# Optimization experiments

Measured on AMD Instinct MI355X. Metric: run time of the kernel, lower is better.

Reference implementation:

```python
import jax, jax.numpy as jnp
import numpy as np

E = 500000       # number of temporal edges
D = 128          # in_feats
DOUT = 128       # out_feats
N_NODES = 50000  # destination node vocabulary


def setup_inputs() -> dict:
    key = jax.random.key(0)
    k = jax.random.split(key, 6)
    src_feat = jax.random.normal(k[0], (E, D), jnp.float32)
    dst_feat = jax.random.normal(k[1], (E, D), jnp.float32)
    # edges sorted by destination node (and implicitly by timestamp within each bucket)
    dst = jnp.sort(jax.random.randint(k[2], (E,), 0, N_NODES))
    W_self = jax.random.normal(k[3], (D, DOUT), jnp.float32) / np.sqrt(D).astype(np.float32)
    b_self = jnp.zeros((DOUT,), jnp.float32)
    W_neigh = jax.random.normal(k[4], (D, DOUT), jnp.float32) / np.sqrt(D).astype(np.float32)
    b_neigh = jnp.zeros((DOUT,), jnp.float32)
    return dict(src_feat=src_feat, dst_feat=dst_feat, dst=dst,
                W_self=W_self, b_self=b_self, W_neigh=W_neigh, b_neigh=b_neigh)


def _segment_cummean(feat, dst):
    """Cumulative mean of `feat` within contiguous buckets of equal `dst`.

    Equivalent to DGL group_apply_edges(group_by='dst') with the 'mean' branch:
    h_feat = cumsum(h_neighs, dim=1) / (deg_index + 1) on the ragged buckets.
    """
    En = feat.shape[0]
    idx = jnp.arange(En)
    is_start = jnp.concatenate([jnp.ones((1,), bool), dst[1:] != dst[:-1]])
    # running max propagates each bucket's start index to all of its edges
    start_idx = jax.lax.associative_scan(jnp.maximum, jnp.where(is_start, idx, 0))
    cs = jnp.cumsum(feat, axis=0)  # [E, D] global prefix sum
    base = jnp.where((start_idx > 0)[:, None],
                     cs[jnp.maximum(start_idx - 1, 0)], jnp.float32(0.0))
    seg_cs = cs - base                       # within-bucket inclusive cumsum
    pos = (idx - start_idx).astype(feat.dtype)
    return seg_cs / (pos + 1.0)[:, None]     # cumulative mean


def reference(src_feat, dst_feat, dst, W_self, b_self, W_neigh, b_neigh):
    h_neigh = _segment_cummean(src_feat, dst)
    # rst = fc_self(h_self) + fc_neigh(mask_feat)
    return (dst_feat @ W_self + b_self) + (h_neigh @ W_neigh + b_neigh)
```

## Files before the change

kernel.cpp:

```cpp
#include <hip/hip_runtime.h>

typedef float f32x4 __attribute__((ext_vector_type(4)));
typedef __bf16 bf16x8 __attribute__((ext_vector_type(8)));

typedef __attribute__((address_space(3))) unsigned char lds_u8;
typedef __attribute__((address_space(1))) const unsigned char g_u8c;

__device__ __forceinline__ unsigned short f2bf(float f) {
  unsigned int u = __float_as_uint(f);
  u += 0x7FFFu + ((u >> 16) & 1u);
  return (unsigned short)(u >> 16);
}
__device__ __forceinline__ unsigned int pk2(float a, float b) {
  return (unsigned int)f2bf(a) | ((unsigned int)f2bf(b) << 16);
}
__device__ __forceinline__ void gload16(const void* g, void* l) {
  __builtin_amdgcn_global_load_lds((g_u8c*)g, (lds_u8*)l, 16, 0, 0);
}

__global__ void k_prep(const float* __restrict__ Ws, const float* __restrict__ Wn,
                       const float* __restrict__ bs, const float* __restrict__ bn,
                       unsigned short* __restrict__ wt, float* __restrict__ bias) {
  int idx = blockIdx.x * 256 + threadIdx.x;
  int n = idx >> 8, k = idx & 255;
  float v = (k < 128) ? Ws[k * 128 + n] : Wn[(k - 128) * 128 + n];
  int ct = n >> 4, l15 = n & 15, kt = k >> 5, lg = (k >> 3) & 3, j = k & 7;
  wt[(((kt << 3) | ct) << 9) + (((lg << 4) | l15) << 3) + j] = f2bf(v);
  if (idx < 128) bias[idx] = bs[idx] + bn[idx];
}

__global__ __launch_bounds__(128, 4) void k_fused(
    const float* __restrict__ src, const float* __restrict__ dstf,
    const int* __restrict__ dst, const unsigned short* __restrict__ wt,
    const float* __restrict__ bias, float* __restrict__ out, int E)
{
  __shared__ __align__(16) unsigned char slab[2][16384];
  const int lane = threadIdx.x & 63, wid = threadIdx.x >> 6;
  const int l15 = lane & 15, lg = lane >> 4;

  const int nwg = gridDim.x, bid = blockIdx.x;
  const int q = nwg >> 3, r = nwg & 7;
  const int xcd = bid & 7, ix = bid >> 3;
  const int swb = (xcd < r ? xcd * (q + 1) : r * (q + 1) + (xcd - r) * q) + ix;

  const long e0 = ((long)swb * 2 + wid) * 16;
  if (e0 >= E) return;
  const long emax = (long)E - 1;
  unsigned char* ssrc = slab[wid];
  unsigned char* sdst = slab[wid] + 8192;

  long drow = e0 + l15; if (drow > emax) drow = emax;
  int myd = dst[drow];
  long back = e0 - 1 - lane;
  long backc = back < 0 ? 0 : back;
  int bd = dst[backc];

  #pragma unroll
  for (int i = 0; i < 8; ++i) {
    int r2 = i * 2 + (lane >> 5);
    long gr = e0 + r2; if (gr > emax) gr = emax;
    int colb = ((lane & 31) << 4) ^ ((r2 & 7) << 5);
    gload16((const char*)src + gr * 512 + colb, ssrc + i * 1024);
  }
  #pragma unroll
  for (int i = 0; i < 8; ++i) {
    int r2 = i * 2 + (lane >> 5);
    long gr = e0 + r2; if (gr > emax) gr = emax;
    int colb = ((lane & 31) << 4) ^ ((r2 & 7) << 5);
    gload16((const char*)dstf + gr * 512 + colb, sdst + i * 1024);
  }

  int d0 = __shfl(myd, 0);
  unsigned long long m = __ballot((back >= 0) && (bd == d0));
  unsigned long long nm = ~m;
  int L = (nm == 0ull) ? 64 : __builtin_ctzll(nm);
  long s = e0 - L;
  while (s > 0 && dst[s - 1] == d0) --s;

  float ax = 0.f, ay = 0.f;
  for (long e = s; e < e0; ++e) {
    float2 v = *(const float2*)(src + e * 128 + lane * 2);
    ax += v.x; ay += v.y;
  }

  asm volatile("s_waitcnt vmcnt(8)" ::: "memory");

  int pos = (int)(e0 - s);
  int prevd = d0;
  #pragma unroll
  for (int rr = 0; rr < 16; ++rr) {
    int d = __shfl(myd, rr);
    if (d != prevd) { ax = 0.f; ay = 0.f; pos = 0; prevd = d; }
    float2 v = *(const float2*)(ssrc + rr * 512 + ((lane * 8) ^ ((rr & 7) << 5)));
    ax += v.x; ay += v.y;
    float inv = __builtin_amdgcn_rcpf((float)(pos + 1));
    *(unsigned int*)(ssrc + rr * 512 + ((lane * 4) ^ ((rr & 7) << 4))) = pk2(ax * inv, ay * inv);
    ++pos;
  }

  asm volatile("s_waitcnt lgkmcnt(0)" ::: "memory");
  asm volatile("s_waitcnt vmcnt(0)" ::: "memory");

  f32x4 acc[8];
  #pragma unroll
  for (int ct = 0; ct < 8; ++ct) acc[ct] = (f32x4){0.f, 0.f, 0.f, 0.f};
  float bcol[8];
  #pragma unroll
  for (int ct = 0; ct < 8; ++ct) bcol[ct] = bias[ct * 16 + l15];

  #pragma unroll
  for (int kt = 0; kt < 8; ++kt) {
    bf16x8 a;
    if (kt < 4) {
      const unsigned char* p = sdst + l15 * 512 + ((kt * 128 + lg * 32) ^ ((l15 & 7) << 5));
      float4 x = *(const float4*)p;
      float4 y = *(const float4*)(p + 16);
      union { unsigned int u[4]; bf16x8 v; } cv;
      cv.u[0] = pk2(x.x, x.y); cv.u[1] = pk2(x.z, x.w);
      cv.u[2] = pk2(y.x, y.y); cv.u[3] = pk2(y.z, y.w);
      a = cv.v;
    } else {
      a = *(const bf16x8*)(ssrc + l15 * 512 + ((((kt - 4) * 64) + lg * 16) ^ ((l15 & 7) << 4)));
    }
    bf16x8 b[8];
    #pragma unroll
    for (int ct = 0; ct < 8; ++ct)
      b[ct] = *(const bf16x8*)(wt + (((kt << 3) | ct) << 9) + (lane << 3));
    #pragma unroll
    for (int ct = 0; ct < 8; ++ct)
      acc[ct] = __builtin_amdgcn_mfma_f32_16x16x32_bf16(a, b[ct], acc[ct], 0, 0, 0);
  }

  #pragma unroll
  for (int i = 0; i < 4; ++i) {
    long row = e0 + lg * 4 + i;
    if (row < E) {
      float* op = out + row * 128 + l15;
      #pragma unroll
      for (int ct = 0; ct < 8; ++ct) op[ct * 16] = acc[ct][i] + bcol[ct];
    }
  }
}

extern "C" void kernel_launch(void* const* d_in, const int* in_sizes, int n_in,
                              void* d_out, int out_size, void* d_ws, size_t ws_size,
                              hipStream_t stream) {
  const float* src_feat = (const float*)d_in[0];
  const float* dst_feat = (const float*)d_in[1];
  const int*   dst      = (const int*)d_in[2];
  const float* W_self   = (const float*)d_in[3];
  const float* b_self   = (const float*)d_in[4];
  const float* W_neigh  = (const float*)d_in[5];
  const float* b_neigh  = (const float*)d_in[6];
  float* out = (float*)d_out;
  const int E = in_sizes[2];

  unsigned short* wt   = (unsigned short*)d_ws;
  float*          bias = (float*)((char*)d_ws + 65536);

  k_prep<<<128, 256, 0, stream>>>(W_self, W_neigh, b_self, b_neigh, wt, bias);

  int blocks = (E + 31) / 32;
  k_fused<<<blocks, 128, 0, stream>>>(src_feat, dst_feat, dst, wt, bias, out, E);
}
```

Measured before the change: 190.5 us.

## Load dst features directly to registers, widen blocks, batch backward prefix loads

Drops the LDS staging of dst_feat rows and loads them straight from global memory into registers just before the MFMA loop. This halves LDS per wave and allows 4 waves per 256-thread block. Bucket-boundary detection becomes a precomputed 16-bit ballot mask instead of per-row shuffles, and the backward prefix accumulation issues loads in batches of eight. In exchange, the dst_feat global loads no longer overlap with the cumulative-mean phase and are read in a less coalesced per-lane pattern, with a full vmcnt(0) wait placed earlier.

```diff
diff --git a/kernel.cpp b/kernel.cpp
--- a/kernel.cpp
+++ b/kernel.cpp
@@ -29,12 +29,12 @@
   if (idx < 128) bias[idx] = bs[idx] + bn[idx];
 }
 
-__global__ __launch_bounds__(128, 4) void k_fused(
+__global__ __launch_bounds__(256, 4) void k_fused(
     const float* __restrict__ src, const float* __restrict__ dstf,
     const int* __restrict__ dst, const unsigned short* __restrict__ wt,
     const float* __restrict__ bias, float* __restrict__ out, int E)
 {
-  __shared__ __align__(16) unsigned char slab[2][16384];
+  __shared__ __align__(16) unsigned char slab[4][8192];
   const int lane = threadIdx.x & 63, wid = threadIdx.x >> 6;
   const int l15 = lane & 15, lg = lane >> 4;
 
@@ -43,14 +43,15 @@
   const int xcd = bid & 7, ix = bid >> 3;
   const int swb = (xcd < r ? xcd * (q + 1) : r * (q + 1) + (xcd - r) * q) + ix;
 
-  const long e0 = ((long)swb * 2 + wid) * 16;
+  const long e0 = ((long)swb * 4 + wid) * 16;
   if (e0 >= E) return;
   const long emax = (long)E - 1;
   unsigned char* ssrc = slab[wid];
-  unsigned char* sdst = slab[wid] + 8192;
 
-  long drow = e0 + l15; if (drow > emax) drow = emax;
-  int myd = dst[drow];
+  long rc = e0 + l15; if (rc > emax) rc = emax;
+  int dcur = dst[rc];
+  long rp = rc - 1; if (rp < 0) rp = 0;
+  int dprev = dst[rp];
   long back = e0 - 1 - lane;
   long backc = back < 0 ? 0 : back;
   int bd = dst[backc];
@@ -62,15 +63,10 @@
     int colb = ((lane & 31) << 4) ^ ((r2 & 7) << 5);
     gload16((const char*)src + gr * 512 + colb, ssrc + i * 1024);
   }
-  #pragma unroll
-  for (int i = 0; i < 8; ++i) {
-    int r2 = i * 2 + (lane >> 5);
-    long gr = e0 + r2; if (gr > emax) gr = emax;
-    int colb = ((lane & 31) << 4) ^ ((r2 & 7) << 5);
-    gload16((const char*)dstf + gr * 512 + colb, sdst + i * 1024);
-  }
 
-  int d0 = __shfl(myd, 0);
+  unsigned mask16 = (unsigned)(__ballot((rc > 0) && (dcur != dprev)) & 0xFFFFull);
+
+  int d0 = __shfl(dcur, 0);
   unsigned long long m = __ballot((back >= 0) && (bd == d0));
   unsigned long long nm = ~m;
   int L = (nm == 0ull) ? 64 : __builtin_ctzll(nm);
@@ -78,19 +74,25 @@
   while (s > 0 && dst[s - 1] == d0) --s;
 
   float ax = 0.f, ay = 0.f;
-  for (long e = s; e < e0; ++e) {
-    float2 v = *(const float2*)(src + e * 128 + lane * 2);
-    ax += v.x; ay += v.y;
+  long e = s;
+  while (e < e0) {
+    int nb = (int)(e0 - e); if (nb > 8) nb = 8;
+    float2 t[8];
+    #pragma unroll
+    for (int j = 0; j < 8; ++j)
+      if (j < nb) t[j] = *(const float2*)(src + (e + j) * 128 + lane * 2);
+    #pragma unroll
+    for (int j = 0; j < 8; ++j)
+      if (j < nb) { ax += t[j].x; ay += t[j].y; }
+    e += nb;
   }
+  int pos = (int)(e0 - s);
 
-  asm volatile("s_waitcnt vmcnt(8)" ::: "memory");
+  asm volatile("s_waitcnt vmcnt(0)" ::: "memory");
 
-  int pos = (int)(e0 - s);
-  int prevd = d0;
   #pragma unroll
   for (int rr = 0; rr < 16; ++rr) {
-    int d = __shfl(myd, rr);
-    if (d != prevd) { ax = 0.f; ay = 0.f; pos = 0; prevd = d; }
+    if (mask16 & (1u << rr)) { ax = 0.f; ay = 0.f; pos = 0; }
     float2 v = *(const float2*)(ssrc + rr * 512 + ((lane * 8) ^ ((rr & 7) << 5)));
     ax += v.x; ay += v.y;
     float inv = __builtin_amdgcn_rcpf((float)(pos + 1));
@@ -99,7 +101,15 @@
   }
 
   asm volatile("s_waitcnt lgkmcnt(0)" ::: "memory");
-  asm volatile("s_waitcnt vmcnt(0)" ::: "memory");
+
+  long arow = e0 + l15; if (arow > emax) arow = emax;
+  const float* ap = dstf + arow * 128 + lg * 8;
+  float4 af[8];
+  #pragma unroll
+  for (int kt = 0; kt < 4; ++kt) {
+    af[kt * 2]     = *(const float4*)(ap + kt * 32);
+    af[kt * 2 + 1] = *(const float4*)(ap + kt * 32 + 4);
+  }
 
   f32x4 acc[8];
   #pragma unroll
@@ -112,9 +122,7 @@
   for (int kt = 0; kt < 8; ++kt) {
     bf16x8 a;
     if (kt < 4) {
-      const unsigned char* p = sdst + l15 * 512 + ((kt * 128 + lg * 32) ^ ((l15 & 7) << 5));
-      float4 x = *(const float4*)p;
-      float4 y = *(const float4*)(p + 16);
+      float4 x = af[kt * 2], y = af[kt * 2 + 1];
       union { unsigned int u[4]; bf16x8 v; } cv;
       cv.u[0] = pk2(x.x, x.y); cv.u[1] = pk2(x.z, x.w);
       cv.u[2] = pk2(y.x, y.y); cv.u[3] = pk2(y.z, y.w);
@@ -160,6 +168,6 @@
 
   k_prep<<<128, 256, 0, stream>>>(W_self, W_neigh, b_self, b_neigh, wt, bias);
 
-  int blocks = (E + 31) / 32;
-  k_fused<<<blocks, 128, 0, stream>>>(src_feat, dst_feat, dst, wt, bias, out, E);
+  int blocks = (E + 63) / 64;
+  k_fused<<<blocks, 256, 0, stream>>>(src_feat, dst_feat, dst, wt, bias, out, E);
 }
```

Result: slower. 212.6 us (+11.5%).
